# Optimization experiments

Measured on AMD Instinct MI355X. Metric: run time of the kernel, lower is better.

## Reference

```python
import jax, jax.numpy as jnp
import numpy as np

# ---- static config (matches init_kwargs) ----
B = 32          # batch
CTX = 128       # context_dim
N_FRAMES = 128
N_SAMPLES = 32768
N_EVENTS = 16
CH = 256        # channels
WIN = 512       # window_size
HOP = WIN // 2  # 256
N_COEFFS = WIN // 2 + 1   # 257
TOTAL_COEFFS = N_COEFFS * 2  # 514


def _hann(n):
    # periodic Hann window (torch.hann_window default)
    i = jnp.arange(n, dtype=jnp.float32)
    return 0.5 * (1.0 - jnp.cos(2.0 * jnp.pi * i / n))


def _forward(param, times, noise, pos, proj_w, proj_b,
             w0, b0, w1, b1, w2, b2, w_out, b_out):
    # proj: [B, CTX] -> [B, CH]
    x = param @ proj_w.T + proj_b
    x = x[:, None, :] + pos                      # [B, N_FRAMES, CH] (pos broadcast)
    # LinearOutputStack: 3 hidden layers w/ leaky_relu(0.2), then output layer
    for w, b in ((w0, b0), (w1, b1), (w2, b2)):
        x = jax.nn.leaky_relu(x @ w.T + b, 0.2)
    x = x @ w_out.T + b_out                      # [B, N_FRAMES, 514]
    x = x.reshape(B, N_FRAMES, N_COEFFS, 2)
    mags = jnp.abs(x[..., 0])                    # [B, F, 257]
    phase = x[..., 1]
    # phase jitter: base phase of ones perturbed by uniform(-1,1) noise
    phase = 1.0 + phase * noise
    # mag/phase recomposition: per-frequency phase increment accumulated over frames
    freqs = jnp.linspace(0.0, 1.0, N_COEFFS)
    p = jnp.cumsum(phase * freqs * jnp.pi, axis=1)
    spec = mags * jnp.exp(1j * p)                # complex [B, F, 257]
    frames = jnp.fft.irfft(spec, n=WIN, axis=-1)  # [B, F, 512]
    frames = frames * _hann(WIN)
    total = (N_FRAMES - 1) * HOP + WIN
    idx = (jnp.arange(N_FRAMES) * HOP)[:, None] + jnp.arange(WIN)  # [F, 512]
    sig = jnp.zeros((B, total), frames.dtype).at[:, idx].add(frames)
    sig = sig[:, :N_SAMPLES]                     # [B, N_SAMPLES]
    # DiracScheduler (pre_sparse): upsample-with-holes frame-resolution diracs
    step = N_SAMPLES // N_FRAMES                 # 256
    up = jnp.zeros((B, N_EVENTS, N_SAMPLES), sig.dtype).at[:, :, ::step].set(times)
    # fft convolve event signal with dirac trains (zero-padded, linear conv)
    n2 = 2 * N_SAMPLES
    S = jnp.fft.rfft(sig, n=n2)[:, None, :]      # [B, 1, n2//2+1]
    T = jnp.fft.rfft(up, n=n2)                   # [B, E, n2//2+1]
    out = jnp.fft.irfft(S * T, n=n2)[..., :N_SAMPLES]
    return out                                   # [B, N_EVENTS, N_SAMPLES]


def setup_inputs() -> dict:
    key = jax.random.key(0)
    ks = jax.random.split(key, 16)
    s = 0.02
    param = jax.random.normal(ks[0], (B, CTX), jnp.float32)
    # sparse dirac times: one event position per (batch, event) at frame resolution
    posn = jax.random.randint(ks[1], (B, N_EVENTS), 0, N_FRAMES)
    amps = jax.random.uniform(ks[2], (B, N_EVENTS), jnp.float32, 0.1, 1.0)
    times = jax.nn.one_hot(posn, N_FRAMES, dtype=jnp.float32) * amps[..., None]
    noise = jax.random.uniform(ks[3], (B, N_FRAMES, N_COEFFS), jnp.float32, -1.0, 1.0)
    pos = jax.random.uniform(ks[4], (1, N_FRAMES, CH), jnp.float32, -0.01, 0.01)
    proj_w = jax.random.normal(ks[5], (CH, CTX), jnp.float32) * s
    proj_b = jnp.zeros((CH,), jnp.float32)
    w0 = jax.random.normal(ks[6], (CH, CH), jnp.float32) * s
    b0 = jnp.zeros((CH,), jnp.float32)
    w1 = jax.random.normal(ks[7], (CH, CH), jnp.float32) * s
    b1 = jnp.zeros((CH,), jnp.float32)
    w2 = jax.random.normal(ks[8], (CH, CH), jnp.float32) * s
    b2 = jnp.zeros((CH,), jnp.float32)
    w_out = jax.random.normal(ks[9], (TOTAL_COEFFS, CH), jnp.float32) * s
    b_out = jnp.zeros((TOTAL_COEFFS,), jnp.float32)
    return dict(param=param, times=times, noise=noise, pos=pos,
                proj_w=proj_w, proj_b=proj_b, w0=w0, b0=b0, w1=w1, b1=b1,
                w2=w2, b2=b2, w_out=w_out, b_out=b_out)


def reference(param, times, noise, pos, proj_w, proj_b,
              w0, b0, w1, b1, w2, b2, w_out, b_out):
    return _forward(param, times, noise, pos, proj_w, proj_b,
                    w0, b0, w1, b1, w2, b2, w_out, b_out)
```

## Files before the change

kernel.cpp:

```cpp
#include <hip/hip_runtime.h>
#include <cstddef>

typedef unsigned short u16;
typedef __bf16 bf16x8 __attribute__((ext_vector_type(8)));
typedef float f32x4 __attribute__((ext_vector_type(4)));

constexpr int B_   = 32;
constexpr int CTX_ = 128;
constexpr int NF_  = 128;
constexpr int NS_  = 32768;
constexpr int NE_  = 16;
constexpr int CH_  = 256;
constexpr int NC_  = 257;
constexpr int TC_  = 514;
constexpr int ROWS_ = B_ * NF_;
constexpr int CHUNK_ = 8;
constexpr int NCH_ = NF_ / CHUNK_;
constexpr int K3MLP_ = 768;
constexpr int SEGM_ = 256;
constexpr int K3IR_ = 960;
constexpr int SEGI_ = 320;
constexpr int PIRW_ = 2 * SEGI_;
constexpr int PMLW_ = 2 * SEGM_;
constexpr float PI_ = 3.14159265358979323846f;

__device__ __forceinline__ float lrelu(float v) { return v > 0.f ? v : 0.2f * v; }
__device__ __forceinline__ u16 f2bf(float x) {
    unsigned u = __float_as_uint(x);
    return (u16)((u + 0x7FFFu + ((u >> 16) & 1u)) >> 16);
}
__device__ __forceinline__ float bf2f(u16 h) { return __uint_as_float(((unsigned)h) << 16); }

__global__ __launch_bounds__(256) void prep_kernel(
    const float* __restrict__ param, const float* __restrict__ pw,
    const float* __restrict__ pb, const float* __restrict__ pos,
    const float* __restrict__ w0, const float* __restrict__ w1,
    const float* __restrict__ w2, const float* __restrict__ wo,
    const float* __restrict__ times,
    u16* __restrict__ Tt, u16* __restrict__ W1p, u16* __restrict__ W2p,
    u16* __restrict__ WOp, int* __restrict__ cnt, float2* __restrict__ taps,
    float* __restrict__ U, float* __restrict__ V)
{
    int blk = blockIdx.x;
    int tid = threadIdx.x;
    if (blk < 1280) {
        __shared__ float lut[512];
        lut[tid]       = cosf((float)tid * (PI_ / 256.f));
        lut[tid + 256] = cosf((float)(tid + 256) * (PI_ / 256.f));
        __syncthreads();
        int idx = blk * 256 + tid;
        int z = idx / (256 * PIRW_);
        int r = idx - z * (256 * PIRW_);
        int n = r / PIRW_, c = r - n * PIRW_;
        bool hiplane = c < SEGI_;
        int j = hiplane ? c : c - SEGI_;
        float val = 0.f;
        if (z == 0) {
            if (j < 129) {
                int k = 2 * j;
                float w = (k == 0 || k == 256) ? 1.f : 2.f;
                int m = (k * n) & 511;
                val = w * (1.f / 512.f) * lut[m];
            } else if (j < 258) {
                int kk = 2 * (j - 129);
                float w = (kk == 0 || kk == 256) ? 1.f : 2.f;
                int m = (kk * n) & 511;
                val = -w * (1.f / 512.f) * lut[(m - 128) & 511];
            }
        } else {
            if (j < 128) {
                int k = 2 * j + 1;
                int m = (k * n) & 511;
                val = 2.f * (1.f / 512.f) * lut[m];
            } else if (j < 256) {
                int kk = 2 * (j - 128) + 1;
                int m = (kk * n) & 511;
                val = -2.f * (1.f / 512.f) * lut[(m - 128) & 511];
            }
        }
        u16 h = f2bf(val);
        Tt[idx] = hiplane ? h : f2bf(val - bf2f(h));
    } else if (blk < 2368) {
        int row = blk - 1280;
        int k = tid;
        float v;
        u16* p;
        if (row < 256) {
            v = w1[row * 256 + k];
            p = W1p + (size_t)row * PMLW_;
        } else if (row < 512) {
            v = w2[(row - 256) * 256 + k];
            p = W2p + (size_t)(row - 256) * PMLW_;
        } else {
            int n = row - 512;
            v = (n < TC_) ? wo[n * 256 + k] : 0.f;
            p = WOp + (size_t)n * PMLW_;
        }
        u16 h = f2bf(v);
        p[k] = h; p[256 + k] = f2bf(v - bf2f(h));
    } else if (blk < 2880) {
        int be = blk - 2368;
        __shared__ int c;
        if (tid == 0) c = 0;
        __syncthreads();
        if (tid < NF_) {
            float v = times[(size_t)be * NF_ + tid];
            if (v != 0.f) {
                int slot = atomicAdd(&c, 1);
                taps[(size_t)be * NF_ + slot] = make_float2((float)tid, v);
            }
        }
        __syncthreads();
        if (tid == 0) cnt[be] = c;
    } else if (blk < 2912) {
        int b = blk - 2880;
        __shared__ float ly[256];
        {
            const float* pr = param + b * CTX_;
            const float* wr = pw + tid * CTX_;
            float s = 0.f;
            #pragma unroll 4
            for (int j = 0; j < CTX_; ++j) s += pr[j] * wr[j];
            ly[tid] = s + pb[tid];
        }
        __syncthreads();
        {
            const float* wn = w0 + tid * CH_;
            float s = 0.f;
            #pragma unroll 4
            for (int c2 = 0; c2 < CH_; ++c2) s += ly[c2] * wn[c2];
            U[b * CH_ + tid] = s;
        }
    } else {
        int f = blk - 2912;
        const float* pf = pos + f * CH_;
        const float* wn = w0 + tid * CH_;
        float s = 0.f;
        #pragma unroll 4
        for (int c2 = 0; c2 < CH_; ++c2) s += pf[c2] * wn[c2];
        V[f * CH_ + tid] = s;
    }
}

__global__ void fuse1_kernel(const float* __restrict__ U, const float* __restrict__ V,
                             const float* __restrict__ b0, u16* __restrict__ Hp) {
    int idx = blockIdx.x * 256 + threadIdx.x;
    int c = idx & 255;
    int row = idx >> 8;
    int b = row >> 7, f = row & 127;
    float v = lrelu(U[b * CH_ + c] + V[f * CH_ + c] + b0[c]);
    u16 h = f2bf(v);
    u16* p = Hp + (size_t)row * PMLW_;
    p[c] = h; p[256 + c] = f2bf(v - bf2f(h));
}

template<int EPI, int K3, int SEG>
__global__ __launch_bounds__(128) void mfgemm(
    const u16* __restrict__ A3, const u16* __restrict__ B3,
    const float* __restrict__ bias, void* __restrict__ Cout,
    int N, int lda, int ldb, int ldc,
    size_t sAz, size_t sBz, size_t sCz)
{
    constexpr int NSTEP = K3 / 64;
    A3 += (size_t)blockIdx.z * sAz;
    B3 += (size_t)blockIdx.z * sBz;
    const int tid = threadIdx.x;
    const int m0 = blockIdx.y * 32, n0 = blockIdx.x * 64;
    __shared__ __align__(16) u16 Als[2 * 32 * 64];
    __shared__ __align__(16) u16 Bls[2 * 64 * 64];
    const int sr = tid >> 2;
    const int sc = (tid & 3) * 16;
    const u16* ga  = A3 + (size_t)(m0 + sr) * lda + sc;
    const u16* gb0 = B3 + (size_t)(n0 + sr) * ldb + sc;
    const u16* gb1 = B3 + (size_t)(n0 + 32 + sr) * ldb + sc;
    const int xr = (sr & 7) << 4;
    const int loA0 = sr * 128 + ((sc * 2) ^ xr);
    const int loA1 = sr * 128 + ((sc * 2 + 16) ^ xr);
    const int loB2 = (sr + 32) * 128 + ((sc * 2) ^ xr);
    const int loB3 = (sr + 32) * 128 + ((sc * 2 + 16) ^ xr);
    const int wv = tid >> 6, lane = tid & 63;
    const int wc = wv * 32;
    const int lr = lane & 15;
    const int lkb = (lane >> 4) * 16;
    const int xf = (lr & 7) << 4;
    const int raf0 = lr * 128, raf1 = (16 + lr) * 128;
    const int rbf0 = (wc + lr) * 128, rbf1 = (wc + 16 + lr) * 128;
    f32x4 acc00 = {0.f, 0.f, 0.f, 0.f}, acc01 = acc00, acc10 = acc00, acc11 = acc00;

    uint4 pa0, pa1, pb0, pb1, pb2, pb3;
    uint4 qa0, qa1, qb0, qb1, qb2, qb3;
    auto kA = [](int kt) { return kt >= 2 * SEG ? kt - 2 * SEG : kt; };
    auto kB = [](int kt) { return kt >= SEG ? kt - SEG : kt; };
    auto loadP = [&](int kt) {
        int a = kA(kt), b = kB(kt);
        pa0 = *(const uint4*)(ga + a);  pa1 = *(const uint4*)(ga + a + 8);
        pb0 = *(const uint4*)(gb0 + b); pb1 = *(const uint4*)(gb0 + b + 8);
        pb2 = *(const uint4*)(gb1 + b); pb3 = *(const uint4*)(gb1 + b + 8);
    };
    auto loadQ = [&](int kt) {
        int a = kA(kt), b = kB(kt);
        qa0 = *(const uint4*)(ga + a);  qa1 = *(const uint4*)(ga + a + 8);
        qb0 = *(const uint4*)(gb0 + b); qb1 = *(const uint4*)(gb0 + b + 8);
        qb2 = *(const uint4*)(gb1 + b); qb3 = *(const uint4*)(gb1 + b + 8);
    };
    auto compute = [&](int p) {
        const char* pa = (const char*)Als + p * 4096;
        const char* pb = (const char*)Bls + p * 8192;
        #pragma unroll
        for (int s = 0; s < 2; ++s) {
            int kb = (s * 64 + lkb) ^ xf;
            bf16x8 a0 = *(const bf16x8*)(pa + raf0 + kb);
            bf16x8 a1 = *(const bf16x8*)(pa + raf1 + kb);
            bf16x8 b0 = *(const bf16x8*)(pb + rbf0 + kb);
            bf16x8 b1 = *(const bf16x8*)(pb + rbf1 + kb);
            acc00 = __builtin_amdgcn_mfma_f32_16x16x32_bf16(a0, b0, acc00, 0, 0, 0);
            acc01 = __builtin_amdgcn_mfma_f32_16x16x32_bf16(a0, b1, acc01, 0, 0, 0);
            acc10 = __builtin_amdgcn_mfma_f32_16x16x32_bf16(a1, b0, acc10, 0, 0, 0);
            acc11 = __builtin_amdgcn_mfma_f32_16x16x32_bf16(a1, b1, acc11, 0, 0, 0);
        }
    };
    auto stage = [&](int p, const uint4& a0, const uint4& a1, const uint4& b0,
                     const uint4& b1, const uint4& b2, const uint4& b3) {
        char* ab = (char*)Als + p * 4096;
        char* bb = (char*)Bls + p * 8192;
        *(uint4*)(ab + loA0) = a0; *(uint4*)(ab + loA1) = a1;
        *(uint4*)(bb + loA0) = b0; *(uint4*)(bb + loA1) = b1;
        *(uint4*)(bb + loB2) = b2; *(uint4*)(bb + loB3) = b3;
    };
    loadP(0);
    if (NSTEP > 1) loadQ(64);
    int p = 0;
    #pragma unroll
    for (int i = 0; i < NSTEP; ++i) {
        if ((i & 1) == 0) {
            stage(p, pa0, pa1, pb0, pb1, pb2, pb3);
            __syncthreads();
            if (i + 2 < NSTEP) loadP((i + 2) * 64);
            compute(p);
        } else {
            stage(p, qa0, qa1, qb0, qb1, qb2, qb3);
            __syncthreads();
            if (i + 2 < NSTEP) loadQ((i + 2) * 64);
            compute(p);
        }
        p ^= 1;
    }
    const int er = (lane >> 4) * 4;
    const int ec = lane & 15;
    auto emit = [&](const f32x4& A, int mi, int ni) {
        #pragma unroll
        for (int r = 0; r < 4; ++r) {
            int m = m0 + mi * 16 + er + r;
            int n = n0 + wc + ni * 16 + ec;
            float v = A[r];
            if (EPI == 0) {
                v = lrelu(v + bias[n]);
                u16 h = f2bf(v);
                u16* p2 = (u16*)Cout + (size_t)m * ldc + n;
                p2[0] = h; p2[256] = f2bf(v - bf2f(h));
            } else if (EPI == 1) {
                if (n < N) ((float*)Cout)[(size_t)m * ldc + n] = v + bias[n];
            } else {
                float* cf = (float*)Cout + (size_t)blockIdx.z * sCz;
                cf[(size_t)m * ldc + n] = v;
            }
        }
    };
    emit(acc00, 0, 0); emit(acc01, 0, 1); emit(acc10, 1, 0); emit(acc11, 1, 1);
}

__global__ void scan1_kernel(const float* __restrict__ raw, const float* __restrict__ noise,
                             double* __restrict__ sums) {
    int b = blockIdx.x, c = blockIdx.y;
    int k = threadIdx.x;
    if (k >= NC_) return;
    float kf = (float)k * (PI_ / 256.f);
    double s = 0.0;
    #pragma unroll
    for (int j = 0; j < CHUNK_; ++j) {
        int row = b * NF_ + c * CHUNK_ + j;
        float2 v = *(const float2*)(raw + (size_t)row * TC_ + 2 * k);
        float d = (1.f + v.y * noise[(size_t)row * NC_ + k]) * kf;
        s += (double)d;
    }
    sums[((size_t)(b * NCH_ + c)) * NC_ + k] = s;
}

__global__ void scan2_kernel(const float* __restrict__ raw, const float* __restrict__ noise,
                             const double* __restrict__ sums,
                             u16* __restrict__ ABe, u16* __restrict__ ABo) {
    int b = blockIdx.x, c = blockIdx.y;
    int k = threadIdx.x;
    if (k >= NC_) {
        int t = k - NC_;
        for (int idx = t; idx < 252; idx += 63) {
            int col;
            u16* base;
            if (idx < 62)       { col = 258 + idx;              base = ABe; }
            else if (idx < 124) { col = SEGI_ + 258 + (idx - 62);  base = ABe; }
            else if (idx < 188) { col = 256 + (idx - 124);       base = ABo; }
            else                { col = SEGI_ + 256 + (idx - 188); base = ABo; }
            for (int j = 0; j < CHUNK_; ++j)
                base[(size_t)(b * NF_ + c * CHUNK_ + j) * PIRW_ + col] = 0;
        }
        return;
    }
    double p = 0.0;
    for (int cc = 0; cc < c; ++cc)
        p += sums[((size_t)(b * NCH_ + cc)) * NC_ + k];
    float kf = (float)k * (PI_ / 256.f);
    int half = k >> 1;
    bool even = (k & 1) == 0;
    int ccol = half;
    int scol = even ? (129 + half) : (128 + half);
    u16* dst = even ? ABe : ABo;
    for (int j = 0; j < CHUNK_; ++j) {
        int row = b * NF_ + c * CHUNK_ + j;
        float2 v = *(const float2*)(raw + (size_t)row * TC_ + 2 * k);
        float d = (1.f + v.y * noise[(size_t)row * NC_ + k]) * kf;
        p += (double)d;
        float m = fabsf(v.x);
        float sn, cs;
        sincosf((float)p, &sn, &cs);
        float a = m * cs, bb = m * sn;
        u16* pr = dst + (size_t)row * PIRW_;
        u16 ha = f2bf(a);
        pr[ccol] = ha; pr[SEGI_ + ccol] = f2bf(a - bf2f(ha));
        u16 hb = f2bf(bb);
        pr[scol] = hb; pr[SEGI_ + scol] = f2bf(bb - bf2f(hb));
    }
}

__global__ __launch_bounds__(256) void conv2_kernel(const float* __restrict__ E,
                                                    const float* __restrict__ O,
                                                    const int* __restrict__ cnt,
                                                    const float2* __restrict__ taps,
                                                    float* __restrict__ out) {
    int be = blockIdx.y;
    int b = be >> 4;
    int n = cnt[be];
    int t = blockIdx.x * 2048 + (int)threadIdx.x * 8;
    int r0 = t & 255;
    float hr[8], hr2[8];
    #pragma unroll
    for (int j = 0; j < 8; ++j) {
        float cj = cosf((float)(r0 + j) * (PI_ / 256.f));
        hr[j]  = 0.5f - 0.5f * cj;
        hr2[j] = 0.5f + 0.5f * cj;
    }
    float acc[8] = {};
    for (int i = 0; i < n; ++i) {
        float2 ka = taps[(size_t)be * NF_ + i];
        int s0 = t - ((int)ka.x << 8);
        if (s0 < 0) continue;
        float amp = ka.y;
        int q = s0 >> 8;
        size_t row = (size_t)(b * NF_ + q) * 256 + r0;
        float4 e0 = *(const float4*)(E + row);
        float4 e1 = *(const float4*)(E + row + 4);
        float4 o0 = *(const float4*)(O + row);
        float4 o1 = *(const float4*)(O + row + 4);
        float sv[8];
        sv[0] = hr[0] * (e0.x + o0.x); sv[1] = hr[1] * (e0.y + o0.y);
        sv[2] = hr[2] * (e0.z + o0.z); sv[3] = hr[3] * (e0.w + o0.w);
        sv[4] = hr[4] * (e1.x + o1.x); sv[5] = hr[5] * (e1.y + o1.y);
        sv[6] = hr[6] * (e1.z + o1.z); sv[7] = hr[7] * (e1.w + o1.w);
        if (q > 0) {
            float4 pe0 = *(const float4*)(E + row - 256);
            float4 pe1 = *(const float4*)(E + row - 252);
            float4 po0 = *(const float4*)(O + row - 256);
            float4 po1 = *(const float4*)(O + row - 252);
            sv[0] += hr2[0] * (pe0.x - po0.x); sv[1] += hr2[1] * (pe0.y - po0.y);
            sv[2] += hr2[2] * (pe0.z - po0.z); sv[3] += hr2[3] * (pe0.w - po0.w);
            sv[4] += hr2[4] * (pe1.x - po1.x); sv[5] += hr2[5] * (pe1.y - po1.y);
            sv[6] += hr2[6] * (pe1.z - po1.z); sv[7] += hr2[7] * (pe1.w - po1.w);
        }
        #pragma unroll
        for (int j = 0; j < 8; ++j) acc[j] += amp * sv[j];
    }
    float* op = out + (size_t)be * NS_ + t;
    *(float4*)op = make_float4(acc[0], acc[1], acc[2], acc[3]);
    *(float4*)(op + 4) = make_float4(acc[4], acc[5], acc[6], acc[7]);
}

extern "C" void kernel_launch(void* const* d_in, const int* in_sizes, int n_in,
                              void* d_out, int out_size, void* d_ws, size_t ws_size,
                              hipStream_t stream) {
    const float* param  = (const float*)d_in[0];
    const float* times  = (const float*)d_in[1];
    const float* noise  = (const float*)d_in[2];
    const float* pos    = (const float*)d_in[3];
    const float* proj_w = (const float*)d_in[4];
    const float* proj_b = (const float*)d_in[5];
    const float* w0 = (const float*)d_in[6];
    const float* b0 = (const float*)d_in[7];
    const float* w1 = (const float*)d_in[8];
    const float* b1 = (const float*)d_in[9];
    const float* w2 = (const float*)d_in[10];
    const float* b2 = (const float*)d_in[11];
    const float* w_out = (const float*)d_in[12];
    const float* b_out = (const float*)d_in[13];
    float* out = (float*)d_out;
    float* ws = (float*)d_ws;

    constexpr size_t U_F    = 32 * 256;
    constexpr size_t V_F    = 128 * 256;
    constexpr size_t HP_F   = (size_t)ROWS_ * PMLW_ / 2;
    constexpr size_t W_F    = (size_t)256 * PMLW_ / 2;
    constexpr size_t WO_F   = (size_t)576 * PMLW_ / 2;
    constexpr size_t RAW_F  = (size_t)ROWS_ * TC_;
    constexpr size_t ABP_F  = 2 * (size_t)ROWS_ * PIRW_ / 2;
    constexpr size_t TTP_F  = 2 * (size_t)256 * PIRW_ / 2;
    constexpr size_t EO_F   = 2 * (size_t)ROWS_ * 256;
    constexpr size_t SUMS_F = (size_t)B_ * NCH_ * NC_ * 2;

    size_t cur = 0;
    float* U    = ws + cur;                 cur += U_F;
    float* V    = ws + cur;                 cur += V_F;
    u16*  H1p   = (u16*)(ws + cur);         cur += HP_F;
    u16*  H2p   = (u16*)(ws + cur);         cur += HP_F;
    u16*  H3p   = (u16*)(ws + cur);         cur += HP_F;
    u16*  W1p   = (u16*)(ws + cur);         cur += W_F;
    u16*  W2p   = (u16*)(ws + cur);         cur += W_F;
    u16*  WOp   = (u16*)(ws + cur);         cur += WO_F;
    float* RAW  = ws + cur;                 cur += RAW_F;
    u16*  ABP   = (u16*)(ws + cur);         cur += ABP_F;
    u16*  ABe   = ABP;
    u16*  ABo   = ABP + (size_t)ROWS_ * PIRW_;
    u16*  TTP   = (u16*)(ws + cur);         cur += TTP_F;
    float* EO   = ws + cur;                 cur += EO_F;
    double* SUMS = (double*)(ws + cur);     cur += SUMS_F;
    int*   CNT  = (int*)(ws + cur);         cur += 512;
    float2* TAPS = (float2*)(ws + cur);

    prep_kernel<<<3040, 256, 0, stream>>>(param, proj_w, proj_b, pos, w0, w1, w2, w_out,
                                          times, TTP, W1p, W2p, WOp, CNT, TAPS, U, V);
    fuse1_kernel<<<ROWS_ * CH_ / 256, 256, 0, stream>>>(U, V, b0, H1p);
    mfgemm<0, K3MLP_, SEGM_><<<dim3(4, 128, 1), 128, 0, stream>>>(H1p, W1p, b1, H2p, 256,
                                                                  PMLW_, PMLW_, PMLW_, 0, 0, 0);
    mfgemm<0, K3MLP_, SEGM_><<<dim3(4, 128, 1), 128, 0, stream>>>(H2p, W2p, b2, H3p, 256,
                                                                  PMLW_, PMLW_, PMLW_, 0, 0, 0);
    mfgemm<1, K3MLP_, SEGM_><<<dim3(9, 128, 1), 128, 0, stream>>>(H3p, WOp, b_out, RAW, TC_,
                                                                  PMLW_, PMLW_, TC_, 0, 0, 0);
    dim3 gS(B_, NCH_);
    scan1_kernel<<<gS, 320, 0, stream>>>(RAW, noise, SUMS);
    scan2_kernel<<<gS, 320, 0, stream>>>(RAW, noise, SUMS, ABe, ABo);
    mfgemm<2, K3IR_, SEGI_><<<dim3(4, 128, 2), 128, 0, stream>>>(ABP, TTP, nullptr, EO, 256,
                                                                 PIRW_, PIRW_, 256,
                                                                 (size_t)ROWS_ * PIRW_,
                                                                 (size_t)256 * PIRW_,
                                                                 (size_t)ROWS_ * 256);
    dim3 gC(NS_ / 2048, B_ * NE_);
    conv2_kernel<<<gC, 256, 0, stream>>>(EO, EO + (size_t)ROWS_ * 256, CNT, TAPS, out);
}
```

Before: 95.11 us.

## Fuse two-pass phase scan into one kernel using shared-memory chunk sums

Replaces the two scan kernels (chunk sums to global doubles, then prefix plus sincos) with a single kernel. Each block handles 16 frequencies across all 128 frames, with 16 chunks of 8 frames each, and exchanges chunk sums through shared memory. This removes one launch, the global sums round trip, and re-reading RAW/noise in the second pass. The cost is a grid of 32x17 blocks where the last block per batch runs one frequency with mostly idle threads, and padding zeroing now loops over all frames per thread. Memory access is strided by frequency groups, so coalescing is weaker.

Measured after the change: 95.62 us. Within noise of the previous version (+0.5%).

```diff
diff --git a/kernel.cpp b/kernel.cpp
--- a/kernel.cpp
+++ b/kernel.cpp
@@ -14,8 +14,6 @@
 constexpr int NC_  = 257;
 constexpr int TC_  = 514;
 constexpr int ROWS_ = B_ * NF_;
-constexpr int CHUNK_ = 8;
-constexpr int NCH_ = NF_ / CHUNK_;
 constexpr int K3MLP_ = 768;
 constexpr int SEGM_ = 256;
 constexpr int K3IR_ = 960;
@@ -269,65 +267,70 @@
     emit(acc00, 0, 0); emit(acc01, 0, 1); emit(acc10, 1, 0); emit(acc11, 1, 1);
 }
 
-__global__ void scan1_kernel(const float* __restrict__ raw, const float* __restrict__ noise,
-                             double* __restrict__ sums) {
-    int b = blockIdx.x, c = blockIdx.y;
-    int k = threadIdx.x;
-    if (k >= NC_) return;
+__global__ __launch_bounds__(256) void scanf_kernel(
+    const float* __restrict__ raw, const float* __restrict__ noise,
+    u16* __restrict__ ABe, u16* __restrict__ ABo)
+{
+    int b = blockIdx.x;
+    int kg = blockIdx.y;
+    int tid = threadIdx.x;
+    int kl = tid & 15;
+    int chunk = tid >> 4;
+    bool active;
+    int k;
+    if (kg < 16) { k = kg * 16 + kl; active = true; }
+    else         { k = 256;          active = (kl == 0); }
+
+    __shared__ double ss[256];
+    float dj[8], mj[8];
+    double s = 0.0;
     float kf = (float)k * (PI_ / 256.f);
-    double s = 0.0;
-    #pragma unroll
-    for (int j = 0; j < CHUNK_; ++j) {
-        int row = b * NF_ + c * CHUNK_ + j;
-        float2 v = *(const float2*)(raw + (size_t)row * TC_ + 2 * k);
-        float d = (1.f + v.y * noise[(size_t)row * NC_ + k]) * kf;
-        s += (double)d;
-    }
-    sums[((size_t)(b * NCH_ + c)) * NC_ + k] = s;
-}
-
-__global__ void scan2_kernel(const float* __restrict__ raw, const float* __restrict__ noise,
-                             const double* __restrict__ sums,
-                             u16* __restrict__ ABe, u16* __restrict__ ABo) {
-    int b = blockIdx.x, c = blockIdx.y;
-    int k = threadIdx.x;
-    if (k >= NC_) {
-        int t = k - NC_;
-        for (int idx = t; idx < 252; idx += 63) {
+    int f0 = chunk * 8;
+    if (active) {
+        #pragma unroll
+        for (int j = 0; j < 8; ++j) {
+            size_t row = (size_t)(b * NF_ + f0 + j);
+            float2 v = *(const float2*)(raw + row * TC_ + 2 * k);
+            dj[j] = (1.f + v.y * noise[row * NC_ + k]) * kf;
+            mj[j] = fabsf(v.x);
+            s += (double)dj[j];
+        }
+    }
+    ss[tid] = s;
+    __syncthreads();
+    if (active) {
+        double p = 0.0;
+        for (int cc = 0; cc < chunk; ++cc)
+            p += ss[cc * 16 + kl];
+        int half = k >> 1;
+        bool even = (k & 1) == 0;
+        int ccol = half;
+        int scol = even ? (129 + half) : (128 + half);
+        u16* dst = even ? ABe : ABo;
+        #pragma unroll
+        for (int j = 0; j < 8; ++j) {
+            p += (double)dj[j];
+            float sn, cs;
+            sincosf((float)p, &sn, &cs);
+            float a = mj[j] * cs, bb = mj[j] * sn;
+            u16* pr = dst + (size_t)(b * NF_ + f0 + j) * PIRW_;
+            u16 ha = f2bf(a);
+            pr[ccol] = ha; pr[SEGI_ + ccol] = f2bf(a - bf2f(ha));
+            u16 hb = f2bf(bb);
+            pr[scol] = hb; pr[SEGI_ + scol] = f2bf(bb - bf2f(hb));
+        }
+    } else {
+        int t = chunk * 15 + kl - 1;
+        for (int idx = t; idx < 252; idx += 240) {
             int col;
             u16* base;
-            if (idx < 62)       { col = 258 + idx;              base = ABe; }
+            if (idx < 62)       { col = 258 + idx;                 base = ABe; }
             else if (idx < 124) { col = SEGI_ + 258 + (idx - 62);  base = ABe; }
-            else if (idx < 188) { col = 256 + (idx - 124);       base = ABo; }
+            else if (idx < 188) { col = 256 + (idx - 124);         base = ABo; }
             else                { col = SEGI_ + 256 + (idx - 188); base = ABo; }
-            for (int j = 0; j < CHUNK_; ++j)
-                base[(size_t)(b * NF_ + c * CHUNK_ + j) * PIRW_ + col] = 0;
-        }
-        return;
-    }
-    double p = 0.0;
-    for (int cc = 0; cc < c; ++cc)
-        p += sums[((size_t)(b * NCH_ + cc)) * NC_ + k];
-    float kf = (float)k * (PI_ / 256.f);
-    int half = k >> 1;
-    bool even = (k & 1) == 0;
-    int ccol = half;
-    int scol = even ? (129 + half) : (128 + half);
-    u16* dst = even ? ABe : ABo;
-    for (int j = 0; j < CHUNK_; ++j) {
-        int row = b * NF_ + c * CHUNK_ + j;
-        float2 v = *(const float2*)(raw + (size_t)row * TC_ + 2 * k);
-        float d = (1.f + v.y * noise[(size_t)row * NC_ + k]) * kf;
-        p += (double)d;
-        float m = fabsf(v.x);
-        float sn, cs;
-        sincosf((float)p, &sn, &cs);
-        float a = m * cs, bb = m * sn;
-        u16* pr = dst + (size_t)row * PIRW_;
-        u16 ha = f2bf(a);
-        pr[ccol] = ha; pr[SEGI_ + ccol] = f2bf(a - bf2f(ha));
-        u16 hb = f2bf(bb);
-        pr[scol] = hb; pr[SEGI_ + scol] = f2bf(bb - bf2f(hb));
+            for (int f = 0; f < NF_; ++f)
+                base[(size_t)(b * NF_ + f) * PIRW_ + col] = 0;
+        }
     }
 }
 
@@ -412,7 +415,6 @@
     constexpr size_t ABP_F  = 2 * (size_t)ROWS_ * PIRW_ / 2;
     constexpr size_t TTP_F  = 2 * (size_t)256 * PIRW_ / 2;
     constexpr size_t EO_F   = 2 * (size_t)ROWS_ * 256;
-    constexpr size_t SUMS_F = (size_t)B_ * NCH_ * NC_ * 2;
 
     size_t cur = 0;
     float* U    = ws + cur;                 cur += U_F;
@@ -429,7 +431,6 @@
     u16*  ABo   = ABP + (size_t)ROWS_ * PIRW_;
     u16*  TTP   = (u16*)(ws + cur);         cur += TTP_F;
     float* EO   = ws + cur;                 cur += EO_F;
-    double* SUMS = (double*)(ws + cur);     cur += SUMS_F;
     int*   CNT  = (int*)(ws + cur);         cur += 512;
     float2* TAPS = (float2*)(ws + cur);
 
@@ -442,9 +443,7 @@
                                                                   PMLW_, PMLW_, PMLW_, 0, 0, 0);
     mfgemm<1, K3MLP_, SEGM_><<<dim3(9, 128, 1), 128, 0, stream>>>(H3p, WOp, b_out, RAW, TC_,
                                                                   PMLW_, PMLW_, TC_, 0, 0, 0);
-    dim3 gS(B_, NCH_);
-    scan1_kernel<<<gS, 320, 0, stream>>>(RAW, noise, SUMS);
-    scan2_kernel<<<gS, 320, 0, stream>>>(RAW, noise, SUMS, ABe, ABo);
+    scanf_kernel<<<dim3(B_, 17), 256, 0, stream>>>(RAW, noise, ABe, ABo);
     mfgemm<2, K3IR_, SEGI_><<<dim3(4, 128, 2), 128, 0, stream>>>(ABP, TTP, nullptr, EO, 256,
                                                                  PIRW_, PIRW_, 256,
                                                                  (size_t)ROWS_ * PIRW_,
```
